# Kernel optimization log

Hardware: AMD Instinct MI355X
Metric: run time of the kernel (lower is better)

## Reference

```python
import jax, jax.numpy as jnp
import numpy as np

N_NODES = 100000
N_EDGES = 1600000


def setup_inputs() -> dict:
    key = jax.random.key(0)
    ks = jax.random.split(key, 5)
    x = jax.random.normal(ks[0], (N_NODES, 128), dtype=jnp.float32)
    edge_index = jax.random.randint(ks[1], (2, N_EDGES), 0, N_NODES, dtype=jnp.int64)
    edge_weight = jnp.ones((N_EDGES,), dtype=jnp.float32)
    W1 = jax.random.normal(ks[2], (128, 128), dtype=jnp.float32) * (1.0 / np.sqrt(128))
    b1 = jnp.zeros((128,), dtype=jnp.float32)
    W2 = jax.random.normal(ks[3], (128, 64), dtype=jnp.float32) * (1.0 / np.sqrt(128))
    b2 = jnp.zeros((64,), dtype=jnp.float32)
    return {"x": x, "edge_index": edge_index, "edge_weight": edge_weight,
            "W1": W1, "b1": b1, "W2": W2, "b2": b2}


def _gcn_conv(x, rows, cols, W, b, n_nodes):
    # GCNConv(normalize=True), unit edge weights (forward overwrites weights with ones)
    h = x @ W                                             # [N, out]
    ones_w = jnp.ones(rows.shape[0], dtype=x.dtype)
    deg = jax.ops.segment_sum(ones_w, cols, num_segments=n_nodes)   # in-degree at targets
    dinv = jnp.where(deg > 0, deg ** -0.5, 0.0)
    norm = dinv[rows] * dinv[cols]                        # [E+N]
    msg = h[rows] * norm[:, None]                         # gather + scale, memory-bound
    out = jax.ops.segment_sum(msg, cols, num_segments=n_nodes)
    return out + b


def reference(x, edge_index, edge_weight, W1, b1, W2, b2):
    n = x.shape[0]
    loop = jnp.arange(n, dtype=edge_index.dtype)
    rows = jnp.concatenate([edge_index[0], loop])         # self-loops (PyG default)
    cols = jnp.concatenate([edge_index[1], loop])
    h = jax.nn.relu(_gcn_conv(x, rows, cols, W1, b1, n))
    logits = _gcn_conv(h, rows, cols, W2, b2, n)
    return logits
```

## Files before the change

### kernel.cpp

```cpp
#include <hip/hip_runtime.h>
#include <hip/hip_fp16.h>


constexpr int NN = 100000;
constexpr int NE = 1600000;
constexpr int BSH = 7;
constexpr int NB = (NN + 127) >> BSH;
constexpr int NBLK = 256;
constexpr int EPB = NE / NBLK;
constexpr int TSTR = 784;

typedef _Float16 f16x8 __attribute__((ext_vector_type(8)));
typedef float f32x4 __attribute__((ext_vector_type(4)));

__global__ __launch_bounds__(256) void k_hist(const int* __restrict__ cols,
                                              int* __restrict__ table) {
  __shared__ int cnt[NB];
  for (int i = threadIdx.x; i < NB; i += 256) cnt[i] = 0;
  __syncthreads();
  int base = blockIdx.x * EPB;
  for (int i = threadIdx.x; i < EPB; i += 256)
    atomicAdd(&cnt[cols[base + i] >> BSH], 1);
  __syncthreads();
  for (int i = threadIdx.x; i < NB; i += 256)
    table[blockIdx.x * TSTR + i] = cnt[i];
}

__global__ __launch_bounds__(256) void k_scanT(const int* __restrict__ table,
                                               int* __restrict__ startOff,
                                               int* __restrict__ btot) {
  __shared__ int s[256];
  int b = blockIdx.x, t = threadIdx.x;
  int v = table[t * TSTR + b];
  s[t] = v;
  __syncthreads();
  for (int off = 1; off < 256; off <<= 1) {
    int tmp = (t >= off) ? s[t - off] : 0;
    __syncthreads();
    s[t] += tmp;
    __syncthreads();
  }
  startOff[t * TSTR + b] = s[t] - v;
  if (t == 255) btot[b] = s[t];
}

__global__ __launch_bounds__(256) void k_scanBkt(const int* __restrict__ btot,
                                                 int* __restrict__ bucketBase) {
  __shared__ int s[256];
  int t = threadIdx.x;
  int base = t * 4;
  int d0 = (base + 0 < NB) ? btot[base + 0] : 0;
  int d1 = (base + 1 < NB) ? btot[base + 1] : 0;
  int d2 = (base + 2 < NB) ? btot[base + 2] : 0;
  int d3 = (base + 3 < NB) ? btot[base + 3] : 0;
  int tsum = d0 + d1 + d2 + d3;
  s[t] = tsum;
  __syncthreads();
  for (int off = 1; off < 256; off <<= 1) {
    int tmp = (t >= off) ? s[t - off] : 0;
    __syncthreads();
    s[t] += tmp;
    __syncthreads();
  }
  int ex = s[t] - tsum;
  if (base + 0 < NB) bucketBase[base + 0] = ex;
  if (base + 1 < NB) bucketBase[base + 1] = ex + d0;
  if (base + 2 < NB) bucketBase[base + 2] = ex + d0 + d1;
  if (base + 3 < NB) bucketBase[base + 3] = ex + d0 + d1 + d2;
}

__global__ __launch_bounds__(256) void k_scat(const int* __restrict__ rows,
                                              const int* __restrict__ cols,
                                              const int* __restrict__ startOff,
                                              const int* __restrict__ bucketBase,
                                              unsigned* __restrict__ binned) {
  __shared__ int scnt[NB];
  int blk = blockIdx.x;
  for (int i = threadIdx.x; i < NB; i += 256)
    scnt[i] = bucketBase[i] + startOff[blk * TSTR + i];
  __syncthreads();
  int base = blk * EPB;
  for (int i = threadIdx.x; i < EPB; i += 256) {
    int c = cols[base + i];
    int r = rows[base + i];
    int pos = atomicAdd(&scnt[c >> BSH], 1);
    binned[pos] = ((unsigned)r << BSH) | (unsigned)(c & 127);
  }
}

__global__ __launch_bounds__(256) void k_fillb(const unsigned* __restrict__ binned,
                                               const int* __restrict__ bucketBase,
                                               const int* __restrict__ btot,
                                               int* __restrict__ rowptr,
                                               int* __restrict__ deg,
                                               float* __restrict__ dinv,
                                               int* __restrict__ srcIdx) {
  __shared__ int cnt[128];
  __shared__ int sc[128];
  __shared__ int rp[128];
  int b = blockIdx.x;
  int nb0 = b << BSH;
  int nn = min(128, NN - nb0);
  int tid = threadIdx.x;
  if (tid < 128) cnt[tid] = 0;
  __syncthreads();
  int ebeg = bucketBase[b];
  int eend = ebeg + btot[b];
  for (int p = ebeg + tid; p < eend; p += 256)
    atomicAdd(&cnt[binned[p] & 127], 1);
  __syncthreads();
  int v = (tid < 128) ? cnt[tid] : 0;
  if (tid < 128) sc[tid] = v;
  __syncthreads();
  for (int off = 1; off < 128; off <<= 1) {
    int tmp = (tid < 128 && tid >= off) ? sc[tid - off] : 0;
    __syncthreads();
    if (tid < 128) sc[tid] += tmp;
    __syncthreads();
  }
  if (tid < 128) {
    int ex = sc[tid] - v;
    rp[tid] = ebeg + ex;
    if (tid < nn) {
      rowptr[nb0 + tid] = ebeg + ex;
      deg[nb0 + tid] = v;
      dinv[nb0 + tid] = rsqrtf((float)v + 1.0f);
    }
    cnt[tid] = 0;
  }
  __syncthreads();
  for (int p = ebeg + tid; p < eend; p += 256) {
    unsigned pk = binned[p];
    int cl = pk & 127;
    int local = atomicAdd(&cnt[cl], 1);
    srcIdx[rp[cl] + local] = (int)(pk >> BSH);
  }
}

__global__ __launch_bounds__(256) void k_wt(const float* __restrict__ W,
                                            __half* __restrict__ Wt, int K, int N) {
  int i = blockIdx.x * 256 + threadIdx.x;
  if (i < K * N) {
    int k = i / N, n = i % N;
    Wt[n * K + k] = __float2half(W[i]);
  }
}

__global__ __launch_bounds__(256) void k_y(const float4* __restrict__ x4,
                                           const float* __restrict__ dinv,
                                           float2* __restrict__ y8) {
  int gid = blockIdx.x * 256 + threadIdx.x;
  if (gid >= NN * 32) return;
  float s = dinv[gid >> 5];
  float4 v = x4[gid];
  union { __half2 h[2]; float2 f; } u;
  u.h[0] = __floats2half2_rn(v.x * s, v.y * s);
  u.h[1] = __floats2half2_rn(v.z * s, v.w * s);
  y8[gid] = u.f;
}

__global__ __launch_bounds__(256) void k_gath1(const __half2* __restrict__ y2,
                                               const int* __restrict__ rowptr,
                                               const int* __restrict__ deg,
                                               const int* __restrict__ srcIdx,
                                               const float* __restrict__ dinv,
                                               __half2* __restrict__ agg) {
  int node = blockIdx.x * 4 + (threadIdx.x >> 6);
  int lane = threadIdx.x & 63;
  if (node >= NN) return;
  int d = deg[node];
  int p = rowptr[node];
  size_t rb = (size_t)node * 64 + lane;
  float2 acc = __half22float2(y2[rb]);
  for (int base = 0; base < d; base += 64) {
    int cnt = min(64, d - base);
    int my = (lane < cnt) ? srcIdx[p + base + lane] : 0;
    int k = 0;
    for (; k + 4 <= cnt; k += 4) {
      int s0 = __shfl(my, k);
      int s1 = __shfl(my, k + 1);
      int s2 = __shfl(my, k + 2);
      int s3 = __shfl(my, k + 3);
      float2 v0 = __half22float2(y2[(size_t)s0 * 64 + lane]);
      float2 v1 = __half22float2(y2[(size_t)s1 * 64 + lane]);
      float2 v2 = __half22float2(y2[(size_t)s2 * 64 + lane]);
      float2 v3 = __half22float2(y2[(size_t)s3 * 64 + lane]);
      acc.x += v0.x + v1.x + v2.x + v3.x;
      acc.y += v0.y + v1.y + v2.y + v3.y;
    }
    for (; k < cnt; k++) {
      int s0 = __shfl(my, k);
      float2 v0 = __half22float2(y2[(size_t)s0 * 64 + lane]);
      acc.x += v0.x;
      acc.y += v0.y;
    }
  }
  float sc = dinv[node];
  agg[rb] = __floats2half2_rn(acc.x * sc, acc.y * sc);
}

__global__ __launch_bounds__(256) void k_gath2(const __half2* __restrict__ z2,
                                               const int* __restrict__ rowptr,
                                               const int* __restrict__ deg,
                                               const int* __restrict__ srcIdx,
                                               const float* __restrict__ dinv,
                                               const float* __restrict__ b2,
                                               float2* __restrict__ out2) {
  int node = blockIdx.x * 8 + (threadIdx.x >> 5);
  int lane = threadIdx.x & 31;
  if (node >= NN) return;
  int d = deg[node];
  int p = rowptr[node];
  float2 acc = __half22float2(z2[(size_t)node * 32 + lane]);
  for (int base = 0; base < d; base += 32) {
    int cnt = min(32, d - base);
    int my = (lane < cnt) ? srcIdx[p + base + lane] : 0;
    int k = 0;
    for (; k + 4 <= cnt; k += 4) {
      int s0 = __shfl(my, k, 32);
      int s1 = __shfl(my, k + 1, 32);
      int s2 = __shfl(my, k + 2, 32);
      int s3 = __shfl(my, k + 3, 32);
      float2 v0 = __half22float2(z2[(size_t)s0 * 32 + lane]);
      float2 v1 = __half22float2(z2[(size_t)s1 * 32 + lane]);
      float2 v2 = __half22float2(z2[(size_t)s2 * 32 + lane]);
      float2 v3 = __half22float2(z2[(size_t)s3 * 32 + lane]);
      acc.x += v0.x + v1.x + v2.x + v3.x;
      acc.y += v0.y + v1.y + v2.y + v3.y;
    }
    for (; k < cnt; k++) {
      int s0 = __shfl(my, k, 32);
      float2 v0 = __half22float2(z2[(size_t)s0 * 32 + lane]);
      acc.x += v0.x;
      acc.y += v0.y;
    }
  }
  float s = dinv[node];
  float2 bv = reinterpret_cast<const float2*>(b2)[lane];
  out2[(size_t)node * 32 + lane] = make_float2(acc.x * s + bv.x, acc.y * s + bv.y);
}

template <int BN, bool BIASRELU, bool ROWSCALE>
__global__ __launch_bounds__(256) void k_gemmM(const __half* __restrict__ A,
                                               const __half* __restrict__ Wt,
                                               const float* __restrict__ bias,
                                               const float* __restrict__ rowscale,
                                               __half* __restrict__ C, int M) {
  constexpr int NT = BN / 16;
  __shared__ __half tile[4][16][BN + 8];
  const int w = threadIdx.x >> 6, l = threadIdx.x & 63;
  const int quad = l >> 4, m = l & 15;
  const int rowTop = blockIdx.x * 64 + w * 16;

  f32x4 acc[NT];
#pragma unroll
  for (int t = 0; t < NT; t++) {
    float bv = BIASRELU ? bias[t * 16 + m] : 0.0f;
    acc[t] = (f32x4){bv, bv, bv, bv};
  }

  int arow = rowTop + m;
  if (arow >= M) arow = M - 1;
  const __half* ap = A + (size_t)arow * 128 + quad * 8;

#pragma unroll
  for (int kc = 0; kc < 128; kc += 32) {
    f16x8 a = *reinterpret_cast<const f16x8*>(ap + kc);
#pragma unroll
    for (int t = 0; t < NT; t++) {
      f16x8 b = *reinterpret_cast<const f16x8*>(
          Wt + (size_t)(t * 16 + m) * 128 + kc + quad * 8);
      acc[t] = __builtin_amdgcn_mfma_f32_16x16x32_f16(a, b, acc[t], 0, 0, 0);
    }
  }

  float rs[4];
  if constexpr (ROWSCALE) {
#pragma unroll
    for (int i = 0; i < 4; i++) {
      int r = rowTop + quad * 4 + i;
      rs[i] = rowscale[r < M ? r : M - 1];
    }
  }
#pragma unroll
  for (int t = 0; t < NT; t++)
#pragma unroll
    for (int i = 0; i < 4; i++) {
      float v = acc[t][i];
      if constexpr (BIASRELU) v = fmaxf(v, 0.0f);
      if constexpr (ROWSCALE) v *= rs[i];
      tile[w][quad * 4 + i][t * 16 + m] = __float2half(v);
    }
  __syncthreads();

  constexpr int CH = 16 * BN / 8;
#pragma unroll
  for (int rep = 0; rep < CH / 64; rep++) {
    int idx = rep * 64 + l;
    int r = idx / (BN / 8), cc = idx % (BN / 8);
    int grow = rowTop + r;
    if (grow < M)
      *reinterpret_cast<float4*>(C + (size_t)grow * BN + cc * 8) =
          *reinterpret_cast<const float4*>(&tile[w][r][cc * 8]);
  }
}

extern "C" void kernel_launch(void* const* d_in, const int* in_sizes, int n_in,
                              void* d_out, int out_size, void* d_ws, size_t ws_size,
                              hipStream_t stream) {
  const float* x  = (const float*)d_in[0];
  const int*   ei = (const int*)d_in[1];
  const int* rows = ei;
  const int* cols = ei + NE;
  const float* W1 = (const float*)d_in[3];
  const float* b1 = (const float*)d_in[4];
  const float* W2 = (const float*)d_in[5];
  const float* b2 = (const float*)d_in[6];
  float* out = (float*)d_out;

  char* base = (char*)d_ws;
  constexpr size_t MB = 1 << 20;
  int*      deg       = (int*)(base + 0 * MB);
  int*      rowptr    = (int*)(base + 1 * MB);
  float*    dinv      = (float*)(base + 2 * MB);
  int*      btot      = (int*)(base + 3 * MB);
  int*      bucketBase= (int*)(base + 3 * MB + 16 * 1024);
  __half*   Wt1       = (__half*)(base + 3 * MB + 64 * 1024);
  __half*   Wt2       = (__half*)(base + 3 * MB + 128 * 1024);
  int*      table     = (int*)(base + 4 * MB);
  int*      startOff  = (int*)(base + 5 * MB);
  unsigned* binned    = (unsigned*)(base + 6 * MB);
  int*      srcIdx    = (int*)(base + 13 * MB);
  __half2*  y         = (__half2*)(base + 20 * MB);
  __half*   aggx      = (__half*)(base + 46 * MB);
  __half*   h1        = (__half*)(base + 72 * MB);
  __half2*  z         = (__half2*)(base + 20 * MB);

  k_wt<<<64, 256, 0, stream>>>(W1, Wt1, 128, 128);
  k_wt<<<32, 256, 0, stream>>>(W2, Wt2, 128, 64);
  k_hist<<<NBLK, 256, 0, stream>>>(cols, table);
  k_scanT<<<NB, 256, 0, stream>>>(table, startOff, btot);
  k_scanBkt<<<1, 256, 0, stream>>>(btot, bucketBase);
  k_scat<<<NBLK, 256, 0, stream>>>(rows, cols, startOff, bucketBase, binned);
  k_fillb<<<NB, 256, 0, stream>>>(binned, bucketBase, btot, rowptr, deg, dinv,
                                  srcIdx);
  k_y<<<(NN * 32 + 255) / 256, 256, 0, stream>>>((const float4*)x, dinv, (float2*)y);
  k_gath1<<<(NN + 3) / 4, 256, 0, stream>>>(y, rowptr, deg, srcIdx, dinv,
                                            (__half2*)aggx);
  k_gemmM<128, true, false><<<(NN + 63) / 64, 256, 0, stream>>>(
      aggx, Wt1, b1, nullptr, h1, NN);
  k_gemmM<64, false, true><<<(NN + 63) / 64, 256, 0, stream>>>(
      h1, Wt2, nullptr, dinv, (__half*)z, NN);
  k_gath2<<<(NN + 7) / 8, 256, 0, stream>>>(z, rowptr, deg, srcIdx, dinv, b2,
                                            (float2*)out);
}
```

Before: 329.9 us.

## Vectorize gather loads with multi-edge wavefronts and fuse scaling into fillb

The two gather kernels now have each wavefront load 16-byte float4 chunks from several source rows at once: 4 edges in parallel for layer 1 and 8 for layer 2. Partial sums are then combined with cross-lane shuffles, replacing the per-lane 4-byte loads that walked one edge at a time. The x-scaling kernel k_y is folded into k_fillb, which reuses its freshly computed dinv from shared memory, and the two weight-transpose launches are merged into one. The aim is more memory-level parallelism and wider transactions in the bandwidth-bound gathers, plus fewer launches, at the cost of shuffle reductions and idle lanes in the final store.

```diff
diff --git a/kernel.cpp b/kernel.cpp
--- a/kernel.cpp
+++ b/kernel.cpp
@@ -91,13 +91,16 @@
 __global__ __launch_bounds__(256) void k_fillb(const unsigned* __restrict__ binned,
                                                const int* __restrict__ bucketBase,
                                                const int* __restrict__ btot,
+                                               const float4* __restrict__ x4,
                                                int* __restrict__ rowptr,
                                                int* __restrict__ deg,
                                                float* __restrict__ dinv,
-                                               int* __restrict__ srcIdx) {
+                                               int* __restrict__ srcIdx,
+                                               float2* __restrict__ y8) {
   __shared__ int cnt[128];
   __shared__ int sc[128];
   __shared__ int rp[128];
+  __shared__ float dnv[128];
   int b = blockIdx.x;
   int nb0 = b << BSH;
   int nn = min(128, NN - nb0);
@@ -121,10 +124,12 @@
   if (tid < 128) {
     int ex = sc[tid] - v;
     rp[tid] = ebeg + ex;
+    float dv = rsqrtf((float)v + 1.0f);
+    dnv[tid] = dv;
     if (tid < nn) {
       rowptr[nb0 + tid] = ebeg + ex;
       deg[nb0 + tid] = v;
-      dinv[nb0 + tid] = rsqrtf((float)v + 1.0f);
+      dinv[nb0 + tid] = dv;
     }
     cnt[tid] = 0;
   }
@@ -135,28 +140,30 @@
     int local = atomicAdd(&cnt[cl], 1);
     srcIdx[rp[cl] + local] = (int)(pk >> BSH);
   }
-}
-
-__global__ __launch_bounds__(256) void k_wt(const float* __restrict__ W,
-                                            __half* __restrict__ Wt, int K, int N) {
+  for (int i = tid; i < nn * 32; i += 256) {
+    int n = i >> 5, j = i & 31;
+    float s = dnv[n];
+    float4 vv = x4[(size_t)(nb0 + n) * 32 + j];
+    union { __half2 h[2]; float2 f; } u;
+    u.h[0] = __floats2half2_rn(vv.x * s, vv.y * s);
+    u.h[1] = __floats2half2_rn(vv.z * s, vv.w * s);
+    y8[(size_t)(nb0 + n) * 32 + j] = u.f;
+  }
+}
+
+__global__ __launch_bounds__(256) void k_wt(const float* __restrict__ W1,
+                                            const float* __restrict__ W2,
+                                            __half* __restrict__ Wt1,
+                                            __half* __restrict__ Wt2) {
   int i = blockIdx.x * 256 + threadIdx.x;
-  if (i < K * N) {
-    int k = i / N, n = i % N;
-    Wt[n * K + k] = __float2half(W[i]);
-  }
-}
-
-__global__ __launch_bounds__(256) void k_y(const float4* __restrict__ x4,
-                                           const float* __restrict__ dinv,
-                                           float2* __restrict__ y8) {
-  int gid = blockIdx.x * 256 + threadIdx.x;
-  if (gid >= NN * 32) return;
-  float s = dinv[gid >> 5];
-  float4 v = x4[gid];
-  union { __half2 h[2]; float2 f; } u;
-  u.h[0] = __floats2half2_rn(v.x * s, v.y * s);
-  u.h[1] = __floats2half2_rn(v.z * s, v.w * s);
-  y8[gid] = u.f;
+  if (i < 128 * 128) {
+    int k = i >> 7, n = i & 127;
+    Wt1[n * 128 + k] = __float2half(W1[i]);
+  } else if (i < 128 * 128 + 128 * 64) {
+    int j = i - 128 * 128;
+    int k = j >> 6, n = j & 63;
+    Wt2[n * 128 + k] = __float2half(W2[j]);
+  }
 }
 
 __global__ __launch_bounds__(256) void k_gath1(const __half2* __restrict__ y2,
@@ -167,36 +174,64 @@
                                                __half2* __restrict__ agg) {
   int node = blockIdx.x * 4 + (threadIdx.x >> 6);
   int lane = threadIdx.x & 63;
-  if (node >= NN) return;
+  int g = lane >> 4, m = lane & 15;
   int d = deg[node];
   int p = rowptr[node];
-  size_t rb = (size_t)node * 64 + lane;
-  float2 acc = __half22float2(y2[rb]);
+  float acc[8];
+#pragma unroll
+  for (int j = 0; j < 8; j++) acc[j] = 0.0f;
+
   for (int base = 0; base < d; base += 64) {
     int cnt = min(64, d - base);
-    int my = (lane < cnt) ? srcIdx[p + base + lane] : 0;
+    int my = srcIdx[min(p + base + lane, NE - 1)];
     int k = 0;
-    for (; k + 4 <= cnt; k += 4) {
-      int s0 = __shfl(my, k);
-      int s1 = __shfl(my, k + 1);
-      int s2 = __shfl(my, k + 2);
-      int s3 = __shfl(my, k + 3);
-      float2 v0 = __half22float2(y2[(size_t)s0 * 64 + lane]);
-      float2 v1 = __half22float2(y2[(size_t)s1 * 64 + lane]);
-      float2 v2 = __half22float2(y2[(size_t)s2 * 64 + lane]);
-      float2 v3 = __half22float2(y2[(size_t)s3 * 64 + lane]);
-      acc.x += v0.x + v1.x + v2.x + v3.x;
-      acc.y += v0.y + v1.y + v2.y + v3.y;
-    }
-    for (; k < cnt; k++) {
-      int s0 = __shfl(my, k);
-      float2 v0 = __half22float2(y2[(size_t)s0 * 64 + lane]);
-      acc.x += v0.x;
-      acc.y += v0.y;
-    }
-  }
-  float sc = dinv[node];
-  agg[rb] = __floats2half2_rn(acc.x * sc, acc.y * sc);
+    for (; k + 8 <= cnt; k += 8) {
+      int s0 = __shfl(my, k + g);
+      int s1 = __shfl(my, k + 4 + g);
+      float4 f0 = *reinterpret_cast<const float4*>(y2 + (size_t)s0 * 64 + m * 4);
+      float4 f1 = *reinterpret_cast<const float4*>(y2 + (size_t)s1 * 64 + m * 4);
+      const __half2* h0 = reinterpret_cast<const __half2*>(&f0);
+      const __half2* h1 = reinterpret_cast<const __half2*>(&f1);
+#pragma unroll
+      for (int q = 0; q < 4; q++) {
+        float2 a = __half22float2(h0[q]);
+        float2 bb = __half22float2(h1[q]);
+        acc[2 * q] += a.x + bb.x;
+        acc[2 * q + 1] += a.y + bb.y;
+      }
+    }
+    for (; k < cnt; k += 4) {
+      int e = k + g;
+      int s0 = __shfl(my, min(e, cnt - 1));
+      if (e < cnt) {
+        float4 f0 = *reinterpret_cast<const float4*>(y2 + (size_t)s0 * 64 + m * 4);
+        const __half2* h0 = reinterpret_cast<const __half2*>(&f0);
+#pragma unroll
+        for (int q = 0; q < 4; q++) {
+          float2 a = __half22float2(h0[q]);
+          acc[2 * q] += a.x;
+          acc[2 * q + 1] += a.y;
+        }
+      }
+    }
+  }
+#pragma unroll
+  for (int j = 0; j < 8; j++) {
+    acc[j] += __shfl_xor(acc[j], 16);
+    acc[j] += __shfl_xor(acc[j], 32);
+  }
+  if (g == 0) {
+    float4 fs = *reinterpret_cast<const float4*>(y2 + (size_t)node * 64 + m * 4);
+    const __half2* hs = reinterpret_cast<const __half2*>(&fs);
+    float sc = dinv[node];
+    union { __half2 h[4]; float4 f; } o;
+#pragma unroll
+    for (int q = 0; q < 4; q++) {
+      float2 a = __half22float2(hs[q]);
+      o.h[q] = __floats2half2_rn((acc[2 * q] + a.x) * sc, (acc[2 * q + 1] + a.y) * sc);
+    }
+    *reinterpret_cast<float4*>(agg + (size_t)node * 64 + m * 4) = o.f;
+  }
 }
 
 __global__ __launch_bounds__(256) void k_gath2(const __half2* __restrict__ z2,
@@ -205,39 +240,71 @@
                                                const int* __restrict__ srcIdx,
                                                const float* __restrict__ dinv,
                                                const float* __restrict__ b2,
-                                               float2* __restrict__ out2) {
-  int node = blockIdx.x * 8 + (threadIdx.x >> 5);
-  int lane = threadIdx.x & 31;
-  if (node >= NN) return;
+                                               float* __restrict__ out) {
+  int node = blockIdx.x * 4 + (threadIdx.x >> 6);
+  int lane = threadIdx.x & 63;
+  int g = lane >> 3, m = lane & 7;
   int d = deg[node];
   int p = rowptr[node];
-  float2 acc = __half22float2(z2[(size_t)node * 32 + lane]);
-  for (int base = 0; base < d; base += 32) {
-    int cnt = min(32, d - base);
-    int my = (lane < cnt) ? srcIdx[p + base + lane] : 0;
+  float acc[8];
+#pragma unroll
+  for (int j = 0; j < 8; j++) acc[j] = 0.0f;
+
+  for (int base = 0; base < d; base += 64) {
+    int cnt = min(64, d - base);
+    int my = srcIdx[min(p + base + lane, NE - 1)];
     int k = 0;
-    for (; k + 4 <= cnt; k += 4) {
-      int s0 = __shfl(my, k, 32);
-      int s1 = __shfl(my, k + 1, 32);
-      int s2 = __shfl(my, k + 2, 32);
-      int s3 = __shfl(my, k + 3, 32);
-      float2 v0 = __half22float2(z2[(size_t)s0 * 32 + lane]);
-      float2 v1 = __half22float2(z2[(size_t)s1 * 32 + lane]);
-      float2 v2 = __half22float2(z2[(size_t)s2 * 32 + lane]);
-      float2 v3 = __half22float2(z2[(size_t)s3 * 32 + lane]);
-      acc.x += v0.x + v1.x + v2.x + v3.x;
-      acc.y += v0.y + v1.y + v2.y + v3.y;
-    }
-    for (; k < cnt; k++) {
-      int s0 = __shfl(my, k, 32);
-      float2 v0 = __half22float2(z2[(size_t)s0 * 32 + lane]);
-      acc.x += v0.x;
-      acc.y += v0.y;
-    }
-  }
-  float s = dinv[node];
-  float2 bv = reinterpret_cast<const float2*>(b2)[lane];
-  out2[(size_t)node * 32 + lane] = make_float2(acc.x * s + bv.x, acc.y * s + bv.y);
+    for (; k + 16 <= cnt; k += 16) {
+      int s0 = __shfl(my, k + g);
+      int s1 = __shfl(my, k + 8 + g);
+      float4 f0 = *reinterpret_cast<const float4*>(z2 + (size_t)s0 * 32 + m * 4);
+      float4 f1 = *reinterpret_cast<const float4*>(z2 + (size_t)s1 * 32 + m * 4);
+      const __half2* h0 = reinterpret_cast<const __half2*>(&f0);
+      const __half2* h1 = reinterpret_cast<const __half2*>(&f1);
+#pragma unroll
+      for (int q = 0; q < 4; q++) {
+        float2 a = __half22float2(h0[q]);
+        float2 bb = __half22float2(h1[q]);
+        acc[2 * q] += a.x + bb.x;
+        acc[2 * q + 1] += a.y + bb.y;
+      }
+    }
+    for (; k < cnt; k += 8) {
+      int e = k + g;
+      int s0 = __shfl(my, min(e, cnt - 1));
+      if (e < cnt) {
+        float4 f0 = *reinterpret_cast<const float4*>(z2 + (size_t)s0 * 32 + m * 4);
+        const __half2* h0 = reinterpret_cast<const __half2*>(&f0);
+#pragma unroll
+        for (int q = 0; q < 4; q++) {
+          float2 a = __half22float2(h0[q]);
+          acc[2 * q] += a.x;
+          acc[2 * q + 1] += a.y;
+        }
+      }
+    }
+  }
+#pragma unroll
+  for (int j = 0; j < 8; j++) {
+    acc[j] += __shfl_xor(acc[j], 8);
+    acc[j] += __shfl_xor(acc[j], 16);
+    acc[j] += __shfl_xor(acc[j], 32);
+  }
+  if (g == 0) {
+    float4 fs = *reinterpret_cast<const float4*>(z2 + (size_t)node * 32 + m * 4);
+    const __half2* hs = reinterpret_cast<const __half2*>(&fs);
+    float s = dinv[node];
+    float4 bv0 = *reinterpret_cast<const float4*>(b2 + m * 8);
+    float4 bv1 = *reinterpret_cast<const float4*>(b2 + m * 8 + 4);
+    float2 a0 = __half22float2(hs[0]), a1 = __half22float2(hs[1]);
+    float2 a2 = __half22float2(hs[2]), a3 = __half22float2(hs[3]);
+    float4 o0 = make_float4((acc[0] + a0.x) * s + bv0.x, (acc[1] + a0.y) * s + bv0.y,
+                            (acc[2] + a1.x) * s + bv0.z, (acc[3] + a1.y) * s + bv0.w);
+    float4 o1 = make_float4((acc[4] + a2.x) * s + bv1.x, (acc[5] + a2.y) * s + bv1.y,
+                            (acc[6] + a3.x) * s + bv1.z, (acc[7] + a3.y) * s + bv1.w);
+    *reinterpret_cast<float4*>(out + (size_t)node * 64 + m * 8) = o0;
+    *reinterpret_cast<float4*>(out + (size_t)node * 64 + m * 8 + 4) = o1;
+  }
 }
 
 template <int BN, bool BIASRELU, bool ROWSCALE>
@@ -336,21 +403,18 @@
   __half*   h1        = (__half*)(base + 72 * MB);
   __half2*  z         = (__half2*)(base + 20 * MB);
 
-  k_wt<<<64, 256, 0, stream>>>(W1, Wt1, 128, 128);
-  k_wt<<<32, 256, 0, stream>>>(W2, Wt2, 128, 64);
+  k_wt<<<96, 256, 0, stream>>>(W1, W2, Wt1, Wt2);
   k_hist<<<NBLK, 256, 0, stream>>>(cols, table);
   k_scanT<<<NB, 256, 0, stream>>>(table, startOff, btot);
   k_scanBkt<<<1, 256, 0, stream>>>(btot, bucketBase);
   k_scat<<<NBLK, 256, 0, stream>>>(rows, cols, startOff, bucketBase, binned);
-  k_fillb<<<NB, 256, 0, stream>>>(binned, bucketBase, btot, rowptr, deg, dinv,
-                                  srcIdx);
-  k_y<<<(NN * 32 + 255) / 256, 256, 0, stream>>>((const float4*)x, dinv, (float2*)y);
-  k_gath1<<<(NN + 3) / 4, 256, 0, stream>>>(y, rowptr, deg, srcIdx, dinv,
-                                            (__half2*)aggx);
+  k_fillb<<<NB, 256, 0, stream>>>(binned, bucketBase, btot, (const float4*)x,
+                                  rowptr, deg, dinv, srcIdx, (float2*)y);
+  k_gath1<<<NN / 4, 256, 0, stream>>>(y, rowptr, deg, srcIdx, dinv,
+                                      (__half2*)aggx);
   k_gemmM<128, true, false><<<(NN + 63) / 64, 256, 0, stream>>>(
       aggx, Wt1, b1, nullptr, h1, NN);
   k_gemmM<64, false, true><<<(NN + 63) / 64, 256, 0, stream>>>(
       h1, Wt2, nullptr, dinv, (__half*)z, NN);
-  k_gath2<<<(NN + 7) / 8, 256, 0, stream>>>(z, rowptr, deg, srcIdx, dinv, b2,
-                                            (float2*)out);
-}
+  k_gath2<<<NN / 4, 256, 0, stream>>>(z, rowptr, deg, srcIdx, dinv, b2, out);
+}
```

After: 331.3 us. No clear change (+0.4%).
